# Performance work log

Measured on AMD Instinct MI355X. Metric: run time of the kernel, lower is better.

## Reference

```python
import jax, jax.numpy as jnp
import numpy as np

# Dims: tokens [B,H,W,C]; 3x3 local window (NB=9 neighbors); relative-pos embed dim RP.
B, H, W, C = 4, 96, 96, 128
K, NB, RP = 3, 9, 8
HID = 128              # edge_hidden_dim = max(hidden_dim//2=128, feature_dim=128)
EDGE_IN = 3 * C + RP   # [center, neighbor, center-neighbor, rel_pos] -> 392
CLIP = 3.0
GATE_EPS = 1e-6
LN_EPS = 1e-5


def _ln(x, w, b):
    m = jnp.mean(x, axis=-1, keepdims=True)
    v = jnp.mean((x - m) ** 2, axis=-1, keepdims=True)
    return (x - m) * jax.lax.rsqrt(v + LN_EPS) * w + b


def _mlp(x, w1, b1, w2, b2):
    # Linear -> GELU (exact/erf, torch default) -> Linear; dropout is identity in eval mode.
    return jax.nn.gelu(x @ w1 + b1, approximate=False) @ w2 + b2


def _eml(drive, resistance, gamma_raw, lam, bias, warmup_eta):
    # EMLUnit energy gate (source not provided; Ohm's-law style drive/resistance,
    # positive resistance via softplus, clipped, warmup-scaled, learned bias).
    gamma = jax.nn.softplus(gamma_raw)
    conduct = drive / (jax.nn.softplus(resistance) + gamma + GATE_EPS)
    return warmup_eta * jnp.clip(lam * conduct, -CLIP, CLIP) + bias


def setup_inputs() -> dict:
    key = jax.random.key(0)
    ks = jax.random.split(key, 8)

    def w(k, shape, std=0.01):
        return jax.random.normal(k, shape, jnp.float32) * std

    return {
        "tokens": jax.random.normal(ks[0], (B, H, W, C), jnp.float32),
        "ln1_w": jnp.ones((C,), jnp.float32), "ln1_b": jnp.zeros((C,), jnp.float32),
        "ln2_w": jnp.ones((C,), jnp.float32), "ln2_b": jnp.zeros((C,), jnp.float32),
        "rel_pos": w(ks[1], (NB, RP), 0.02),
        "d_w1": w(ks[2], (EDGE_IN, HID)), "d_b1": jnp.zeros((HID,), jnp.float32),
        "d_w2": w(ks[3], (HID, 1)), "d_b2": jnp.zeros((1,), jnp.float32),
        "r_w1": w(ks[4], (EDGE_IN, HID)), "r_b1": jnp.zeros((HID,), jnp.float32),
        "r_w2": w(ks[5], (HID, 1)), "r_b2": jnp.zeros((1,), jnp.float32),
        "v_w": w(ks[6], (C, C)), "v_b": jnp.zeros((C,), jnp.float32),
        "o_w": w(ks[7], (C, C)), "o_b": jnp.zeros((C,), jnp.float32),
        "eml_gamma": jnp.full((1,), 0.1, jnp.float32),
        "eml_lam": jnp.ones((1,), jnp.float32),
        "eml_bias": jnp.full((1,), -0.3, jnp.float32),
    }


def reference(tokens, ln1_w, ln1_b, ln2_w, ln2_b, rel_pos,
              d_w1, d_b1, d_w2, d_b2, r_w1, r_b1, r_w2, r_b2,
              v_w, v_b, o_w, o_b, eml_gamma, eml_lam, eml_bias):
    b, h, w_, c = tokens.shape
    hw = h * w_
    norm = _ln(tokens, ln1_w, ln1_b)
    # nn.Unfold(kernel=3, padding=1): zero-pad then gather 3x3 windows (row-major ky,kx order).
    pad = jnp.pad(norm, ((0, 0), (1, 1), (1, 1), (0, 0)))
    neigh = jnp.stack([pad[:, dy:dy + h, dx:dx + w_, :]
                       for dy in range(K) for dx in range(K)], axis=3)  # [B,H,W,9,C]
    neigh = neigh.reshape(b, hw, NB, c)
    center = jnp.broadcast_to(norm.reshape(b, hw, 1, c), (b, hw, NB, c))
    relp = jnp.broadcast_to(rel_pos[None, None], (b, hw, NB, RP))
    edge = jnp.concatenate([center, neigh, center - neigh, relp], axis=-1)  # [B,HW,9,392]
    drive = _mlp(edge, d_w1, d_b1, d_w2, d_b2)[..., 0]        # [B,HW,9]
    resistance = _mlp(edge, r_w1, r_b1, r_w2, r_b2)[..., 0]   # [B,HW,9]
    energy = _eml(drive, resistance, eml_gamma, eml_lam, eml_bias, 1.0)
    gate = jax.nn.sigmoid(energy)[..., None]                  # [B,HW,9,1]
    values = neigh @ v_w + v_b                                # [B,HW,9,C]
    gate_mass = jnp.clip(jnp.sum(gate, axis=2), GATE_EPS, None)  # [B,HW,1]
    message = jnp.sum(gate * values, axis=2) / gate_mass      # [B,HW,C]
    update = (message @ o_w + o_b).reshape(b, h, w_, c)
    return _ln(tokens + update, ln2_w, ln2_b)
```

## Files before the change

kernel.cpp:

```cpp
#include <hip/hip_runtime.h>
#include <stdint.h>

#define NPIX 36864

using bf16x8 = __attribute__((ext_vector_type(8))) short;
using f32x4  = __attribute__((ext_vector_type(4))) float;
using f32x2  = __attribute__((ext_vector_type(2))) float;

__device__ __forceinline__ float bf2f(uint16_t u){
  return __uint_as_float(((uint32_t)u) << 16);
}
__device__ __forceinline__ float bl(uint32_t u){ return __uint_as_float(u << 16); }
__device__ __forceinline__ float bh(uint32_t u){ return __uint_as_float(u & 0xFFFF0000u); }
__device__ __forceinline__ uint16_t f2bf(float f){
  uint32_t u = __float_as_uint(f);
  u += 0x7fffu + ((u >> 16) & 1u);
  return (uint16_t)(u >> 16);
}
__device__ __forceinline__ float ldw(const void* p, int i, bool f32){
  return f32 ? ((const float*)p)[i] : bf2f(((const uint16_t*)p)[i]);
}
__device__ __forceinline__ bool probe_f32(const void* ones_vec){
  return ((const uint32_t*)ones_vec)[0] == 0x3F800000u;
}
__device__ __forceinline__ float softplusf(float x){
  return fmaxf(x, 0.f) + __logf(1.f + __expf(-fabsf(x)));
}
__device__ __forceinline__ f32x2 up2(uint32_t u){
  f32x2 r; r.x = __uint_as_float(u << 16); r.y = __uint_as_float(u & 0xFFFF0000u); return r;
}
__device__ __forceinline__ void sg2(f32x2& acc, uint32_t c, uint32_t n, f32x2 r, f32x2 w){
  f32x2 z = up2(c) + up2(n) + r;
  float sx = __builtin_amdgcn_fmed3f(fmaf(z.x, 0.4255f, 0.5f), 0.f, 1.f);
  float sy = __builtin_amdgcn_fmed3f(fmaf(z.y, 0.4255f, 0.5f), 0.f, 1.f);
  acc.x = fmaf(z.x * sx, w.x, acc.x);
  acc.y = fmaf(z.y * sy, w.y, acc.y);
}

#define LIDX(p, ch) ((p)*128 + ((((ch) >> 3) ^ ((p) & 15)) << 3) + ((ch) & 7))

__global__ __launch_bounds__(256) void pre_kernel(const void* __restrict__ tokens,
                            const void* __restrict__ ln1w, const void* __restrict__ ln1b,
                            const void* __restrict__ dw1, const void* __restrict__ rw1,
                            const void* __restrict__ vw,  const void* __restrict__ relp,
                            const void* __restrict__ db1, const void* __restrict__ rb1,
                            const void* __restrict__ ow,
                            const void* __restrict__ dw2, const void* __restrict__ rw2,
                            const void* __restrict__ vb,  const void* __restrict__ db2,
                            const void* __restrict__ rb2, const void* __restrict__ eg,
                            const void* __restrict__ el,  const void* __restrict__ eb,
                            uint16_t* __restrict__ norm,
                            uint16_t* __restrict__ wcatT, float* __restrict__ Rd,
                            float* __restrict__ Rr, uint16_t* __restrict__ owT,
                            float* __restrict__ w2df, float* __restrict__ w2rf,
                            float* __restrict__ vbf, float* __restrict__ sc){
  const bool F = probe_f32(ln1w);
  const int b = blockIdx.x;
  if (b < NPIX/4){
    const int wv = threadIdx.x >> 6, lane = threadIdx.x & 63;
    const int p = b * 4 + wv;
    float f0, f1;
    if (F){
      const float2 t = ((const float2*)tokens)[(size_t)p*64 + lane];
      f0 = t.x; f1 = t.y;
    } else {
      const uint32_t pk = ((const uint32_t*)tokens)[(size_t)p*64 + lane];
      f0 = bl(pk); f1 = bh(pk);
    }
    float s = f0 + f1;
    #pragma unroll
    for (int m = 1; m < 64; m <<= 1) s += __shfl_xor(s, m, 64);
    const float mean = s * (1.f/128.f);
    const float d0 = f0 - mean, d1 = f1 - mean;
    float q = d0*d0 + d1*d1;
    #pragma unroll
    for (int m = 1; m < 64; m <<= 1) q += __shfl_xor(q, m, 64);
    const float rs = rsqrtf(q * (1.f/128.f) + 1e-5f);
    const float n0 = d0*rs*ldw(ln1w, 2*lane, F)   + ldw(ln1b, 2*lane, F);
    const float n1 = d1*rs*ldw(ln1w, 2*lane+1, F) + ldw(ln1b, 2*lane+1, F);
    ((uint32_t*)(norm + (size_t)p*128))[lane] = (uint32_t)f2bf(n0) | ((uint32_t)f2bf(n1) << 16);
    return;
  }
  const int j = (b - NPIX/4) * 2 + (threadIdx.x >> 7);
  const int c = threadIdx.x & 127;
  if (j < 640){
    float val;
    if (j < 128)      val = ldw(dw1, c*128 + j, F)             + ldw(dw1, (256+c)*128 + j, F);
    else if (j < 256) val = ldw(dw1, (128+c)*128 + (j-128), F) - ldw(dw1, (256+c)*128 + (j-128), F);
    else if (j < 384) val = ldw(rw1, c*128 + (j-256), F)       + ldw(rw1, (256+c)*128 + (j-256), F);
    else if (j < 512) val = ldw(rw1, (128+c)*128 + (j-384), F) - ldw(rw1, (256+c)*128 + (j-384), F);
    else              val = ldw(vw, c*128 + (j-512), F);
    wcatT[j*128 + c] = f2bf(val);
  } else if (j < 649){
    const int k = j - 640;
    float sd = ldw(db1, c, F);
    float sr = ldw(rb1, c, F);
    #pragma unroll
    for (int r = 0; r < 8; ++r){
      float rp = ldw(relp, k*8 + r, F);
      sd += rp * ldw(dw1, (384+r)*128 + c, F);
      sr += rp * ldw(rw1, (384+r)*128 + c, F);
    }
    Rd[k*128 + c] = sd;
    Rr[k*128 + c] = sr;
  } else if (j < 777){
    const int n = j - 649;
    owT[n*128 + c] = f2bf(ldw(ow, c*128 + n, F));
  } else {
    w2df[c] = ldw(dw2, c, F);
    w2rf[c] = ldw(rw2, c, F);
    vbf[c]  = ldw(vb, c, F);
    if (c == 0){
      sc[0] = ldw(db2, 0, F);
      sc[1] = ldw(rb2, 0, F);
      sc[2] = softplusf(ldw(eg, 0, F));
      sc[3] = ldw(el, 0, F);
      sc[4] = ldw(eb, 0, F);
    }
  }
}

__global__ __launch_bounds__(256) void gemm1_kernel(const uint16_t* __restrict__ A,
                                                    const uint16_t* __restrict__ BT,
                                                    uint16_t* __restrict__ PT,
                                                    uint16_t* __restrict__ V){
  __shared__ __align__(16) char smem[49152];
  uint16_t* As = (uint16_t*)smem;
  uint16_t* Bs = (uint16_t*)(smem + 16384);
  const int row0 = blockIdx.x * 64;
  const int s    = blockIdx.y;
  const int t = threadIdx.x;
  #pragma unroll
  for (int i = 0; i < 4; ++i){
    const int cid = t + i*256;
    const int r = cid >> 4, c8 = cid & 15;
    *(uint4*)&As[r*128 + ((c8 ^ (r & 15)) << 3)] = *(const uint4*)&A[(size_t)(row0+r)*128 + c8*8];
  }
  #pragma unroll
  for (int i = 0; i < 8; ++i){
    const int cid = t + i*256;
    const int r = cid >> 4, c8 = cid & 15;
    *(uint4*)&Bs[r*128 + ((c8 ^ (r & 15)) << 3)] = *(const uint4*)&BT[(size_t)(s*128 + r)*128 + c8*8];
  }
  __syncthreads();
  const int wv = t >> 6, lane = t & 63;
  const int wc = wv * 32;
  const int lr = lane & 15, quad = lane >> 4;
  f32x4 acc[4][2] = {};
  #pragma unroll
  for (int kk = 0; kk < 4; ++kk){
    const int chunk = kk*4 + quad;
    bf16x8 a[4], b[2];
    #pragma unroll
    for (int mi = 0; mi < 4; ++mi){
      const int r = mi*16 + lr;
      a[mi] = *(const bf16x8*)&As[r*128 + ((chunk ^ (r & 15)) << 3)];
    }
    #pragma unroll
    for (int ni = 0; ni < 2; ++ni){
      const int r = wc + ni*16 + lr;
      b[ni] = *(const bf16x8*)&Bs[r*128 + ((chunk ^ (r & 15)) << 3)];
    }
    #pragma unroll
    for (int mi = 0; mi < 4; ++mi)
      #pragma unroll
      for (int ni = 0; ni < 2; ++ni)
        acc[mi][ni] = __builtin_amdgcn_mfma_f32_16x16x32_bf16(a[mi], b[ni], acc[mi][ni], 0, 0, 0);
  }
  __syncthreads();
  #pragma unroll
  for (int mi = 0; mi < 4; ++mi){
    #pragma unroll
    for (int ni = 0; ni < 2; ++ni){
      const int ch   = wc + ni*16 + lr;
      const int rowb = mi*16 + quad*4;
      #pragma unroll
      for (int r = 0; r < 4; ++r)
        As[LIDX(rowb + r, ch)] = f2bf(acc[mi][ni][r]);
    }
  }
  __syncthreads();
  uint16_t* const dst = (s == 4) ? V : (PT + (size_t)s * NPIX * 128);
  #pragma unroll
  for (int i = 0; i < 4; ++i){
    const int idx = t + i*256;
    const int c8 = idx & 15, p = idx >> 4;
    const uint4 v = *(const uint4*)&As[p*128 + ((c8 ^ (p & 15)) << 3)];
    ((uint4*)dst)[(size_t)(row0 + p)*16 + c8] = v;
  }
}

__global__ __launch_bounds__(576) void emsg_kernel(
    const uint16_t* __restrict__ PT, const uint16_t* __restrict__ Vg,
    const float* __restrict__ Rd, const float* __restrict__ Rr,
    const float* __restrict__ w2df, const float* __restrict__ w2rf,
    const float* __restrict__ sc, const float* __restrict__ vbf,
    uint16_t* __restrict__ msg){
  __shared__ __align__(16) char smem[79104];
  uint16_t* const PnD = (uint16_t*)smem;
  uint16_t* const PnR = (uint16_t*)(smem + 25600);
  uint16_t* const Vl  = (uint16_t*)(smem + 51200);
  float*    const gl  = (float*)  (smem + 76800);

  const int bid = blockIdx.x;
  const int b   = bid / 144;
  const int tl  = bid - b*144;
  const int ty  = tl / 12;
  const int y0  = ty * 8;
  const int x0  = (tl - ty*12) * 8;
  const int tid = threadIdx.x;

  const uint16_t* const P1 = PT + (size_t)NPIX*128;
  const uint16_t* const P3 = PT + (size_t)3*NPIX*128;

  for (int i = tid; i < 4800; i += 576){
    const int arr = i / 1600;
    const int rem = i - arr*1600;
    const int hq  = rem >> 4;
    const int ch  = rem & 15;
    const int hy  = hq / 10;
    const int hx  = hq - hy*10;
    const int y = y0 - 1 + hy, x = x0 - 1 + hx;
    uint4 v = {0u, 0u, 0u, 0u};
    if (((unsigned)y < 96u) && ((unsigned)x < 96u)){
      const size_t pg = (size_t)((b*96 + y)*96 + x);
      const uint16_t* src = (arr == 0 ? P1 : (arr == 1 ? P3 : Vg)) + pg*128 + ch*8;
      v = *(const uint4*)src;
    }
    if (arr == 2){
      *(uint4*)&Vl[hq*128 + ch*8] = v;
    } else {
      uint16_t* const d = (arr == 0) ? PnD : PnR;
      *(uint4*)((char*)d + hq*256 + ((ch ^ (hq & 15)) << 4)) = v;
    }
  }
  __syncthreads();

  const int wv = tid >> 6, lane = tid & 63;
  const int k  = __builtin_amdgcn_readfirstlane(wv);
  const int ky = k / 3, kx = k - ky*3;
  const int py = lane >> 3, px = lane & 7;
  const int hq = (py + ky)*10 + (px + kx);
  const size_t pg = (size_t)((b*96 + y0 + py)*96 + (x0 + px));
  const float sc0 = sc[0], sc1 = sc[1], sc2 = sc[2], sc3 = sc[3], sc4 = sc[4];
  const char* const nbD = (const char*)PnD + hq*256;
  const char* const nbR = (const char*)PnR + hq*256;
  const int hsw = hq & 15;

  f32x2 ad = {0.f, 0.f};
  {
    const uint4*  Cp = (const uint4*)(PT + pg*128);
    const float4* r4 = (const float4*)(Rd + k*128);
    const float4* w4 = (const float4*)w2df;
    uint4 c = Cp[0];
    uint4 n = *(const uint4*)(nbD + ((0 ^ hsw) << 4));
    #pragma unroll
    for (int i = 0; i < 16; ++i){
      uint4 cn, nn;
      if (i < 15){
        cn = Cp[i+1];
        nn = *(const uint4*)(nbD + (((i+1) ^ hsw) << 4));
      }
      const float4 rA = r4[2*i], rB = r4[2*i+1];
      const float4 wA = w4[2*i], wB = w4[2*i+1];
      sg2(ad, c.x, n.x, f32x2{rA.x, rA.y}, f32x2{wA.x, wA.y});
      sg2(ad, c.y, n.y, f32x2{rA.z, rA.w}, f32x2{wA.z, wA.w});
      sg2(ad, c.z, n.z, f32x2{rB.x, rB.y}, f32x2{wB.x, wB.y});
      sg2(ad, c.w, n.w, f32x2{rB.z, rB.w}, f32x2{wB.z, wB.w});
      c = cn; n = nn;
    }
  }
  f32x2 ar = {0.f, 0.f};
  {
    const uint4*  Cp = (const uint4*)(PT + (size_t)2*NPIX*128 + pg*128);
    const float4* r4 = (const float4*)(Rr + k*128);
    const float4* w4 = (const float4*)w2rf;
    uint4 c = Cp[0];
    uint4 n = *(const uint4*)(nbR + ((0 ^ hsw) << 4));
    #pragma unroll
    for (int i = 0; i < 16; ++i){
      uint4 cn, nn;
      if (i < 15){
        cn = Cp[i+1];
        nn = *(const uint4*)(nbR + (((i+1) ^ hsw) << 4));
      }
      const float4 rA = r4[2*i], rB = r4[2*i+1];
      const float4 wA = w4[2*i], wB = w4[2*i+1];
      sg2(ar, c.x, n.x, f32x2{rA.x, rA.y}, f32x2{wA.x, wA.y});
      sg2(ar, c.y, n.y, f32x2{rA.z, rA.w}, f32x2{wA.z, wA.w});
      sg2(ar, c.z, n.z, f32x2{rB.x, rB.y}, f32x2{wB.x, wB.y});
      sg2(ar, c.w, n.w, f32x2{rB.z, rB.w}, f32x2{wB.z, wB.w});
      c = cn; n = nn;
    }
  }
  const float drive  = (ad.x + ad.y) + sc0;
  const float resist = (ar.x + ar.y) + sc1;
  const float cond = __fdividef(drive, softplusf(resist) + sc2 + 1e-6f);
  const float en = fminf(fmaxf(sc3 * cond, -3.0f), 3.0f) + sc4;
  const float e = __expf(-en);
  gl[k*64 + lane] = __builtin_amdgcn_rcpf(1.0f + e);
  __syncthreads();

  if (wv < 8){
    const float2 vb2 = ((const float2*)vbf)[lane];
    #pragma unroll
    for (int j = 0; j < 8; ++j){
      const int m  = wv*8 + j;
      const int my = m >> 3, mx = m & 7;
      float gk[9], gsum = 0.f;
      #pragma unroll
      for (int kk = 0; kk < 9; ++kk){ gk[kk] = gl[kk*64 + m]; gsum += gk[kk]; }
      float a0 = 0.f, a1 = 0.f;
      #pragma unroll
      for (int kk = 0; kk < 9; ++kk){
        const int kyy = kk / 3;
        const int h2  = (my + kyy)*10 + (mx + kk - kyy*3);
        const uint32_t u = ((const uint32_t*)Vl)[h2*64 + lane];
        a0 = fmaf(gk[kk], bl(u), a0);
        a1 = fmaf(gk[kk], bh(u), a1);
      }
      const float inv = __fdividef(1.0f, fmaxf(gsum, 1e-6f));
      a0 = (a0 + gsum * vb2.x) * inv;
      a1 = (a1 + gsum * vb2.y) * inv;
      const size_t p2 = (size_t)((b*96 + y0 + my)*96 + (x0 + mx));
      ((uint32_t*)msg)[p2*64 + lane] = (uint32_t)f2bf(a0) | ((uint32_t)f2bf(a1) << 16);
    }
  }
}

__global__ __launch_bounds__(256) void out_kernel(const uint16_t* __restrict__ Amsg,
    const uint16_t* __restrict__ owT, const void* __restrict__ tokens,
    const void* __restrict__ ob,  const void* __restrict__ ln2w,
    const void* __restrict__ ln2b, void* __restrict__ out){
  const bool F = probe_f32(ln2w);
  __shared__ __align__(16) char smem[49152];
  uint16_t* Bs = (uint16_t*)smem;
  uint16_t* As = (uint16_t*)(smem + 32768);
  float*    U  = (float*)smem;
  const int row0 = blockIdx.x * 64;
  const int t = threadIdx.x;
  const int wv = t >> 6, lane = t & 63;
  #pragma unroll
  for (int i = 0; i < 8; ++i){
    const int cid = t + i*256;
    const int r = cid >> 4, c8 = cid & 15;
    *(uint4*)&Bs[r*128 + ((c8 ^ (r & 15)) << 3)] = *(const uint4*)&owT[(size_t)r*128 + c8*8];
  }
  #pragma unroll
  for (int i = 0; i < 4; ++i){
    const int cid = t + i*256;
    const int r = cid >> 4, c8 = cid & 15;
    *(uint4*)&As[r*128 + ((c8 ^ (r & 15)) << 3)] = *(const uint4*)&Amsg[(size_t)(row0+r)*128 + c8*8];
  }
  __syncthreads();
  const int wc = wv * 32;
  const int lr = lane & 15, quad = lane >> 4;
  f32x4 acc[4][2] = {};
  #pragma unroll
  for (int kk = 0; kk < 4; ++kk){
    const int chunk = kk*4 + quad;
    bf16x8 a[4], b[2];
    #pragma unroll
    for (int mi = 0; mi < 4; ++mi){
      const int r = mi*16 + lr;
      a[mi] = *(const bf16x8*)&As[r*128 + ((chunk ^ (r & 15)) << 3)];
    }
    #pragma unroll
    for (int ni = 0; ni < 2; ++ni){
      const int r = wc + ni*16 + lr;
      b[ni] = *(const bf16x8*)&Bs[r*128 + ((chunk ^ (r & 15)) << 3)];
    }
    #pragma unroll
    for (int mi = 0; mi < 4; ++mi)
      #pragma unroll
      for (int ni = 0; ni < 2; ++ni)
        acc[mi][ni] = __builtin_amdgcn_mfma_f32_16x16x32_bf16(a[mi], b[ni], acc[mi][ni], 0, 0, 0);
  }
  __syncthreads();
  #pragma unroll
  for (int mi = 0; mi < 4; ++mi)
    #pragma unroll
    for (int ni = 0; ni < 2; ++ni)
      #pragma unroll
      for (int r = 0; r < 4; ++r)
        U[(mi*16 + quad*4 + r)*128 + wc + ni*16 + lr] = acc[mi][ni][r];
  __syncthreads();
  const float lw0 = ldw(ln2w, 2*lane, F), lw1 = ldw(ln2w, 2*lane+1, F);
  const float lb0 = ldw(ln2b, 2*lane, F), lb1 = ldw(ln2b, 2*lane+1, F);
  const float ob0 = ldw(ob, 2*lane, F),   ob1 = ldw(ob, 2*lane+1, F);
  for (int j = 0; j < 16; ++j){
    const int row = wv*16 + j;
    const int p = row0 + row;
    const float2 uv = ((const float2*)U)[row*64 + lane];
    float t0, t1;
    if (F){
      const float2 tk = ((const float2*)tokens)[(size_t)p*64 + lane];
      t0 = tk.x; t1 = tk.y;
    } else {
      const uint32_t tk = ((const uint32_t*)tokens)[(size_t)p*64 + lane];
      t0 = bl(tk); t1 = bh(tk);
    }
    const float a0 = uv.x + ob0 + t0;
    const float a1 = uv.y + ob1 + t1;
    float s = a0 + a1;
    #pragma unroll
    for (int m = 1; m < 64; m <<= 1) s += __shfl_xor(s, m, 64);
    const float mean = s * (1.f/128.f);
    const float d0 = a0 - mean, d1 = a1 - mean;
    float q = d0*d0 + d1*d1;
    #pragma unroll
    for (int m = 1; m < 64; m <<= 1) q += __shfl_xor(q, m, 64);
    const float rs = rsqrtf(q * (1.f/128.f) + 1e-5f);
    const float o0 = d0*rs*lw0 + lb0;
    const float o1 = d1*rs*lw1 + lb1;
    if (F){
      ((float2*)out)[(size_t)p*64 + lane] = make_float2(o0, o1);
    } else {
      ((uint32_t*)out)[(size_t)p*64 + lane] = (uint32_t)f2bf(o0) | ((uint32_t)f2bf(o1) << 16);
    }
  }
}

extern "C" void kernel_launch(void* const* d_in, const int* in_sizes, int n_in,
                              void* d_out, int out_size, void* d_ws, size_t ws_size,
                              hipStream_t stream) {
  const void* tokens = d_in[0];
  const void* ln1w   = d_in[1];
  const void* ln1b   = d_in[2];
  const void* ln2w   = d_in[3];
  const void* ln2b   = d_in[4];
  const void* relp   = d_in[5];
  const void* dw1    = d_in[6];
  const void* db1    = d_in[7];
  const void* dw2    = d_in[8];
  const void* db2    = d_in[9];
  const void* rw1    = d_in[10];
  const void* rb1    = d_in[11];
  const void* rw2    = d_in[12];
  const void* rb2    = d_in[13];
  const void* vw     = d_in[14];
  const void* vb     = d_in[15];
  const void* ow     = d_in[16];
  const void* ob     = d_in[17];
  const void* eg     = d_in[18];
  const void* el     = d_in[19];
  const void* eb     = d_in[20];

  char* ws = (char*)d_ws;
  uint16_t* normb = (uint16_t*)(ws + 0);
  uint16_t* PT    = (uint16_t*)(ws + 9437184);
  uint16_t* V     = (uint16_t*)(ws + 47185920);
  uint16_t* wcatT = (uint16_t*)(ws + 57950208);
  float*    Rd    = (float*)   (ws + 58114048);
  float*    Rr    = (float*)   (ws + 58118656);
  uint16_t* owT   = (uint16_t*)(ws + 58123264);
  float*    w2df  = (float*)   (ws + 58156032);
  float*    w2rf  = (float*)   (ws + 58156544);
  float*    vbf   = (float*)   (ws + 58157056);
  float*    sc    = (float*)   (ws + 58157568);
  uint16_t* msg   = normb;

  pre_kernel<<<NPIX/4 + 389, 256, 0, stream>>>(tokens, ln1w, ln1b,
                                       dw1, rw1, vw, relp, db1, rb1, ow,
                                       dw2, rw2, vb, db2, rb2, eg, el, eb,
                                       normb, wcatT, Rd, Rr, owT, w2df, w2rf, vbf, sc);
  gemm1_kernel<<<dim3(NPIX/64, 5), 256, 0, stream>>>(normb, wcatT, PT, V);
  emsg_kernel<<<576, 576, 0, stream>>>(PT, V, Rd, Rr, w2df, w2rf, sc, vbf, msg);
  out_kernel<<<NPIX/64, 256, 0, stream>>>(msg, owT, tokens, ob, ln2w, ln2b, d_out);
}
```

Baseline: 193.8 us.

## Loop gemm1 over all weight slices per block; read emsg neighbours directly from global

gemm1 now loads the activation tile once and loops over the five weight slices inside a single block, instead of launching a 2D grid that reloads the A tile for every slice. It uses a separate LDS region for the output staging. emsg_kernel no longer stages the neighbour projections in LDS. Each group of 8 lanes handles one pixel, with each lane covering 16 channels, reads centre and neighbour projections straight from global memory, zero-masks out-of-bounds neighbours, and reduces with shuffles. The V halo loads are issued early into registers, and the much smaller LDS footprint allows more resident blocks; the cost is 9x redundant global/L2 reads of the neighbour rows.

```diff
diff --git a/kernel.cpp b/kernel.cpp
--- a/kernel.cpp
+++ b/kernel.cpp
@@ -35,6 +35,9 @@
   float sy = __builtin_amdgcn_fmed3f(fmaf(z.y, 0.4255f, 0.5f), 0.f, 1.f);
   acc.x = fmaf(z.x * sx, w.x, acc.x);
   acc.y = fmaf(z.y * sy, w.y, acc.y);
+}
+__device__ __forceinline__ uint4 m4(uint4 v, uint32_t m){
+  v.x &= m; v.y &= m; v.z &= m; v.w &= m; return v;
 }
 
 #define LIDX(p, ch) ((p)*128 + ((((ch) >> 3) ^ ((p) & 15)) << 3) + ((ch) & 7))
@@ -124,83 +127,82 @@
                                                     const uint16_t* __restrict__ BT,
                                                     uint16_t* __restrict__ PT,
                                                     uint16_t* __restrict__ V){
-  __shared__ __align__(16) char smem[49152];
+  __shared__ __align__(16) char smem[65536];
   uint16_t* As = (uint16_t*)smem;
   uint16_t* Bs = (uint16_t*)(smem + 16384);
+  uint16_t* Cs = (uint16_t*)(smem + 49152);
   const int row0 = blockIdx.x * 64;
-  const int s    = blockIdx.y;
   const int t = threadIdx.x;
+  const int wv = t >> 6, lane = t & 63;
+  const int wc = wv * 32;
+  const int lr = lane & 15, quad = lane >> 4;
   #pragma unroll
   for (int i = 0; i < 4; ++i){
     const int cid = t + i*256;
     const int r = cid >> 4, c8 = cid & 15;
     *(uint4*)&As[r*128 + ((c8 ^ (r & 15)) << 3)] = *(const uint4*)&A[(size_t)(row0+r)*128 + c8*8];
   }
-  #pragma unroll
-  for (int i = 0; i < 8; ++i){
-    const int cid = t + i*256;
-    const int r = cid >> 4, c8 = cid & 15;
-    *(uint4*)&Bs[r*128 + ((c8 ^ (r & 15)) << 3)] = *(const uint4*)&BT[(size_t)(s*128 + r)*128 + c8*8];
-  }
-  __syncthreads();
-  const int wv = t >> 6, lane = t & 63;
-  const int wc = wv * 32;
-  const int lr = lane & 15, quad = lane >> 4;
-  f32x4 acc[4][2] = {};
-  #pragma unroll
-  for (int kk = 0; kk < 4; ++kk){
-    const int chunk = kk*4 + quad;
-    bf16x8 a[4], b[2];
+  for (int s = 0; s < 5; ++s){
+    #pragma unroll
+    for (int i = 0; i < 8; ++i){
+      const int cid = t + i*256;
+      const int r = cid >> 4, c8 = cid & 15;
+      *(uint4*)&Bs[r*128 + ((c8 ^ (r & 15)) << 3)] = *(const uint4*)&BT[(size_t)(s*128 + r)*128 + c8*8];
+    }
+    __syncthreads();
+    f32x4 acc[4][2] = {};
+    #pragma unroll
+    for (int kk = 0; kk < 4; ++kk){
+      const int chunk = kk*4 + quad;
+      bf16x8 a[4], b[2];
+      #pragma unroll
+      for (int mi = 0; mi < 4; ++mi){
+        const int r = mi*16 + lr;
+        a[mi] = *(const bf16x8*)&As[r*128 + ((chunk ^ (r & 15)) << 3)];
+      }
+      #pragma unroll
+      for (int ni = 0; ni < 2; ++ni){
+        const int r = wc + ni*16 + lr;
+        b[ni] = *(const bf16x8*)&Bs[r*128 + ((chunk ^ (r & 15)) << 3)];
+      }
+      #pragma unroll
+      for (int mi = 0; mi < 4; ++mi)
+        #pragma unroll
+        for (int ni = 0; ni < 2; ++ni)
+          acc[mi][ni] = __builtin_amdgcn_mfma_f32_16x16x32_bf16(a[mi], b[ni], acc[mi][ni], 0, 0, 0);
+    }
     #pragma unroll
     for (int mi = 0; mi < 4; ++mi){
-      const int r = mi*16 + lr;
-      a[mi] = *(const bf16x8*)&As[r*128 + ((chunk ^ (r & 15)) << 3)];
-    }
-    #pragma unroll
-    for (int ni = 0; ni < 2; ++ni){
-      const int r = wc + ni*16 + lr;
-      b[ni] = *(const bf16x8*)&Bs[r*128 + ((chunk ^ (r & 15)) << 3)];
-    }
-    #pragma unroll
-    for (int mi = 0; mi < 4; ++mi)
-      #pragma unroll
-      for (int ni = 0; ni < 2; ++ni)
-        acc[mi][ni] = __builtin_amdgcn_mfma_f32_16x16x32_bf16(a[mi], b[ni], acc[mi][ni], 0, 0, 0);
-  }
-  __syncthreads();
-  #pragma unroll
-  for (int mi = 0; mi < 4; ++mi){
-    #pragma unroll
-    for (int ni = 0; ni < 2; ++ni){
-      const int ch   = wc + ni*16 + lr;
-      const int rowb = mi*16 + quad*4;
-      #pragma unroll
-      for (int r = 0; r < 4; ++r)
-        As[LIDX(rowb + r, ch)] = f2bf(acc[mi][ni][r]);
-    }
-  }
-  __syncthreads();
-  uint16_t* const dst = (s == 4) ? V : (PT + (size_t)s * NPIX * 128);
-  #pragma unroll
-  for (int i = 0; i < 4; ++i){
-    const int idx = t + i*256;
-    const int c8 = idx & 15, p = idx >> 4;
-    const uint4 v = *(const uint4*)&As[p*128 + ((c8 ^ (p & 15)) << 3)];
-    ((uint4*)dst)[(size_t)(row0 + p)*16 + c8] = v;
-  }
-}
-
-__global__ __launch_bounds__(576) void emsg_kernel(
+      #pragma unroll
+      for (int ni = 0; ni < 2; ++ni){
+        const int ch   = wc + ni*16 + lr;
+        const int rowb = mi*16 + quad*4;
+        #pragma unroll
+        for (int r = 0; r < 4; ++r)
+          Cs[LIDX(rowb + r, ch)] = f2bf(acc[mi][ni][r]);
+      }
+    }
+    __syncthreads();
+    uint16_t* const dst = (s == 4) ? V : (PT + (size_t)s * NPIX * 128);
+    #pragma unroll
+    for (int i = 0; i < 4; ++i){
+      const int idx = t + i*256;
+      const int c8 = idx & 15, p = idx >> 4;
+      const uint4 v = *(const uint4*)&Cs[p*128 + ((c8 ^ (p & 15)) << 3)];
+      ((uint4*)dst)[(size_t)(row0 + p)*16 + c8] = v;
+    }
+  }
+}
+
+__global__ __launch_bounds__(576, 5) void emsg_kernel(
     const uint16_t* __restrict__ PT, const uint16_t* __restrict__ Vg,
     const float* __restrict__ Rd, const float* __restrict__ Rr,
     const float* __restrict__ w2df, const float* __restrict__ w2rf,
     const float* __restrict__ sc, const float* __restrict__ vbf,
     uint16_t* __restrict__ msg){
-  __shared__ __align__(16) char smem[79104];
-  uint16_t* const PnD = (uint16_t*)smem;
-  uint16_t* const PnR = (uint16_t*)(smem + 25600);
-  uint16_t* const Vl  = (uint16_t*)(smem + 51200);
-  float*    const gl  = (float*)  (smem + 76800);
+  __shared__ __align__(16) char smem[27904];
+  uint16_t* const Vl = (uint16_t*)smem;
+  float*    const gl = (float*)(smem + 25600);
 
   const int bid = blockIdx.x;
   const int b   = bid / 144;
@@ -210,106 +212,115 @@
   const int x0  = (tl - ty*12) * 8;
   const int tid = threadIdx.x;
 
-  const uint16_t* const P1 = PT + (size_t)NPIX*128;
-  const uint16_t* const P3 = PT + (size_t)3*NPIX*128;
-
-  for (int i = tid; i < 4800; i += 576){
-    const int arr = i / 1600;
-    const int rem = i - arr*1600;
-    const int hq  = rem >> 4;
-    const int ch  = rem & 15;
-    const int hy  = hq / 10;
-    const int hx  = hq - hy*10;
-    const int y = y0 - 1 + hy, x = x0 - 1 + hx;
-    uint4 v = {0u, 0u, 0u, 0u};
-    if (((unsigned)y < 96u) && ((unsigned)x < 96u)){
-      const size_t pg = (size_t)((b*96 + y)*96 + x);
-      const uint16_t* src = (arr == 0 ? P1 : (arr == 1 ? P3 : Vg)) + pg*128 + ch*8;
-      v = *(const uint4*)src;
-    }
-    if (arr == 2){
-      *(uint4*)&Vl[hq*128 + ch*8] = v;
-    } else {
-      uint16_t* const d = (arr == 0) ? PnD : PnR;
-      *(uint4*)((char*)d + hq*256 + ((ch ^ (hq & 15)) << 4)) = v;
-    }
-  }
-  __syncthreads();
+  uint4 sv0 = {0,0,0,0}, sv1 = {0,0,0,0}, sv2 = {0,0,0,0};
+  const bool has2 = (tid + 1152) < 1600;
+  {
+    const int i0 = tid, i1 = tid + 576, i2 = tid + 1152;
+    #define LDV(dst, i) { \
+      const int hq = (i) >> 4, ch = (i) & 15; \
+      const int hy = hq / 10, hx = hq - hy*10; \
+      const int y = y0 - 1 + hy, x = x0 - 1 + hx; \
+      if (((unsigned)y < 96u) && ((unsigned)x < 96u)) \
+        dst = *(const uint4*)&Vg[((size_t)((b*96 + y)*96 + x))*128 + ch*8]; }
+    LDV(sv0, i0)
+    LDV(sv1, i1)
+    if (has2) LDV(sv2, i2)
+    #undef LDV
+  }
 
   const int wv = tid >> 6, lane = tid & 63;
   const int k  = __builtin_amdgcn_readfirstlane(wv);
   const int ky = k / 3, kx = k - ky*3;
-  const int py = lane >> 3, px = lane & 7;
-  const int hq = (py + ky)*10 + (px + kx);
-  const size_t pg = (size_t)((b*96 + y0 + py)*96 + (x0 + px));
+  const int dy = ky - 1, dx = kx - 1;
+  const int pl = lane >> 3;
+  const int cg = lane & 7;
   const float sc0 = sc[0], sc1 = sc[1], sc2 = sc[2], sc3 = sc[3], sc4 = sc[4];
-  const char* const nbD = (const char*)PnD + hq*256;
-  const char* const nbR = (const char*)PnR + hq*256;
-  const int hsw = hq & 15;
-
-  f32x2 ad = {0.f, 0.f};
+
+  float4 RD[4], WD[4];
   {
-    const uint4*  Cp = (const uint4*)(PT + pg*128);
-    const float4* r4 = (const float4*)(Rd + k*128);
-    const float4* w4 = (const float4*)w2df;
-    uint4 c = Cp[0];
-    uint4 n = *(const uint4*)(nbD + ((0 ^ hsw) << 4));
-    #pragma unroll
-    for (int i = 0; i < 16; ++i){
-      uint4 cn, nn;
-      if (i < 15){
-        cn = Cp[i+1];
-        nn = *(const uint4*)(nbD + (((i+1) ^ hsw) << 4));
-      }
-      const float4 rA = r4[2*i], rB = r4[2*i+1];
-      const float4 wA = w4[2*i], wB = w4[2*i+1];
-      sg2(ad, c.x, n.x, f32x2{rA.x, rA.y}, f32x2{wA.x, wA.y});
-      sg2(ad, c.y, n.y, f32x2{rA.z, rA.w}, f32x2{wA.z, wA.w});
-      sg2(ad, c.z, n.z, f32x2{rB.x, rB.y}, f32x2{wB.x, wB.y});
-      sg2(ad, c.w, n.w, f32x2{rB.z, rB.w}, f32x2{wB.z, wB.w});
-      c = cn; n = nn;
-    }
-  }
-  f32x2 ar = {0.f, 0.f};
+    const float4* r4 = (const float4*)(Rd + k*128) + cg*4;
+    const float4* w4 = (const float4*)w2df + cg*4;
+    #pragma unroll
+    for (int i = 0; i < 4; ++i){ RD[i] = r4[i]; WD[i] = w4[i]; }
+  }
+  const float4* const r4r = (const float4*)(Rr + k*128) + cg*4;
+  const float4* const w4r = (const float4*)w2rf + cg*4;
+
+  const uint4* const S0 = (const uint4*)PT;
+  const uint4* const S1 = (const uint4*)(PT + (size_t)NPIX*128);
+  const uint4* const S2 = (const uint4*)(PT + (size_t)2*NPIX*128);
+  const uint4* const S3 = (const uint4*)(PT + (size_t)3*NPIX*128);
+
+  const int xn = x0 + pl + dx;
+  const bool xin = ((unsigned)xn < 96u);
+
+  for (int ry = 0; ry < 8; ++ry){
+    const int y = y0 + ry;
+    const int p = (b*96 + y)*96 + x0 + pl;
+    const int yn = y + dy;
+    const bool inb = xin && ((unsigned)yn < 96u);
+    const uint32_t m = inb ? 0xFFFFFFFFu : 0u;
+    const int q = inb ? ((b*96 + yn)*96 + xn) : p;
+    const size_t cb = (size_t)p*16 + cg*2;
+    const size_t nb = (size_t)q*16 + cg*2;
+    const uint4 c0a = S0[cb],   c0b = S0[cb+1];
+    const uint4 n1a = m4(S1[nb], m), n1b = m4(S1[nb+1], m);
+    const uint4 c2a = S2[cb],   c2b = S2[cb+1];
+    const uint4 n3a = m4(S3[nb], m), n3b = m4(S3[nb+1], m);
+
+    f32x2 ad = {0.f, 0.f};
+    sg2(ad, c0a.x, n1a.x, f32x2{RD[0].x, RD[0].y}, f32x2{WD[0].x, WD[0].y});
+    sg2(ad, c0a.y, n1a.y, f32x2{RD[0].z, RD[0].w}, f32x2{WD[0].z, WD[0].w});
+    sg2(ad, c0a.z, n1a.z, f32x2{RD[1].x, RD[1].y}, f32x2{WD[1].x, WD[1].y});
+    sg2(ad, c0a.w, n1a.w, f32x2{RD[1].z, RD[1].w}, f32x2{WD[1].z, WD[1].w});
+    sg2(ad, c0b.x, n1b.x, f32x2{RD[2].x, RD[2].y}, f32x2{WD[2].x, WD[2].y});
+    sg2(ad, c0b.y, n1b.y, f32x2{RD[2].z, RD[2].w}, f32x2{WD[2].z, WD[2].w});
+    sg2(ad, c0b.z, n1b.z, f32x2{RD[3].x, RD[3].y}, f32x2{WD[3].x, WD[3].y});
+    sg2(ad, c0b.w, n1b.w, f32x2{RD[3].z, RD[3].w}, f32x2{WD[3].z, WD[3].w});
+
+    const float4 RRa = r4r[0], RRb = r4r[1], RRc = r4r[2], RRd = r4r[3];
+    const float4 WRa = w4r[0], WRb = w4r[1], WRc = w4r[2], WRd = w4r[3];
+    f32x2 ar = {0.f, 0.f};
+    sg2(ar, c2a.x, n3a.x, f32x2{RRa.x, RRa.y}, f32x2{WRa.x, WRa.y});
+    sg2(ar, c2a.y, n3a.y, f32x2{RRa.z, RRa.w}, f32x2{WRa.z, WRa.w});
+    sg2(ar, c2a.z, n3a.z, f32x2{RRb.x, RRb.y}, f32x2{WRb.x, WRb.y});
+    sg2(ar, c2a.w, n3a.w, f32x2{RRb.z, RRb.w}, f32x2{WRb.z, WRb.w});
+    sg2(ar, c2b.x, n3b.x, f32x2{RRc.x, RRc.y}, f32x2{WRc.x, WRc.y});
+    sg2(ar, c2b.y, n3b.y, f32x2{RRc.z, RRc.w}, f32x2{WRc.z, WRc.w});
+    sg2(ar, c2b.z, n3b.z, f32x2{RRd.x, RRd.y}, f32x2{WRd.x, WRd.y});
+    sg2(ar, c2b.w, n3b.w, f32x2{RRd.z, RRd.w}, f32x2{WRd.z, WRd.w});
+
+    float sd = ad.x + ad.y;
+    float sr = ar.x + ar.y;
+    sd += __shfl_xor(sd, 1, 64); sd += __shfl_xor(sd, 2, 64); sd += __shfl_xor(sd, 4, 64);
+    sr += __shfl_xor(sr, 1, 64); sr += __shfl_xor(sr, 2, 64); sr += __shfl_xor(sr, 4, 64);
+
+    const float drive  = sd + sc0;
+    const float resist = sr + sc1;
+    const float cond = __fdividef(drive, softplusf(resist) + sc2 + 1e-6f);
+    const float en = fminf(fmaxf(sc3 * cond, -3.0f), 3.0f) + sc4;
+    const float e = __expf(-en);
+    const float g = __builtin_amdgcn_rcpf(1.0f + e);
+    if (cg == 0) gl[k*64 + ry*8 + pl] = g;
+  }
+
   {
-    const uint4*  Cp = (const uint4*)(PT + (size_t)2*NPIX*128 + pg*128);
-    const float4* r4 = (const float4*)(Rr + k*128);
-    const float4* w4 = (const float4*)w2rf;
-    uint4 c = Cp[0];
-    uint4 n = *(const uint4*)(nbR + ((0 ^ hsw) << 4));
-    #pragma unroll
-    for (int i = 0; i < 16; ++i){
-      uint4 cn, nn;
-      if (i < 15){
-        cn = Cp[i+1];
-        nn = *(const uint4*)(nbR + (((i+1) ^ hsw) << 4));
-      }
-      const float4 rA = r4[2*i], rB = r4[2*i+1];
-      const float4 wA = w4[2*i], wB = w4[2*i+1];
-      sg2(ar, c.x, n.x, f32x2{rA.x, rA.y}, f32x2{wA.x, wA.y});
-      sg2(ar, c.y, n.y, f32x2{rA.z, rA.w}, f32x2{wA.z, wA.w});
-      sg2(ar, c.z, n.z, f32x2{rB.x, rB.y}, f32x2{wB.x, wB.y});
-      sg2(ar, c.w, n.w, f32x2{rB.z, rB.w}, f32x2{wB.z, wB.w});
-      c = cn; n = nn;
-    }
-  }
-  const float drive  = (ad.x + ad.y) + sc0;
-  const float resist = (ar.x + ar.y) + sc1;
-  const float cond = __fdividef(drive, softplusf(resist) + sc2 + 1e-6f);
-  const float en = fminf(fmaxf(sc3 * cond, -3.0f), 3.0f) + sc4;
-  const float e = __expf(-en);
-  gl[k*64 + lane] = __builtin_amdgcn_rcpf(1.0f + e);
+    const int i0 = tid, i1 = tid + 576, i2 = tid + 1152;
+    *(uint4*)&Vl[(i0 >> 4)*128 + (i0 & 15)*8] = sv0;
+    *(uint4*)&Vl[(i1 >> 4)*128 + (i1 & 15)*8] = sv1;
+    if (has2) *(uint4*)&Vl[(i2 >> 4)*128 + (i2 & 15)*8] = sv2;
+  }
   __syncthreads();
 
   if (wv < 8){
     const float2 vb2 = ((const float2*)vbf)[lane];
     #pragma unroll
     for (int j = 0; j < 8; ++j){
-      const int m  = wv*8 + j;
-      const int my = m >> 3, mx = m & 7;
+      const int mp = wv*8 + j;
+      const int my = mp >> 3, mx = mp & 7;
       float gk[9], gsum = 0.f;
       #pragma unroll
-      for (int kk = 0; kk < 9; ++kk){ gk[kk] = gl[kk*64 + m]; gsum += gk[kk]; }
+      for (int kk = 0; kk < 9; ++kk){ gk[kk] = gl[kk*64 + mp]; gsum += gk[kk]; }
       float a0 = 0.f, a1 = 0.f;
       #pragma unroll
       for (int kk = 0; kk < 9; ++kk){
@@ -464,7 +475,7 @@
                                        dw1, rw1, vw, relp, db1, rb1, ow,
                                        dw2, rw2, vb, db2, rb2, eg, el, eb,
                                        normb, wcatT, Rd, Rr, owT, w2df, w2rf, vbf, sc);
-  gemm1_kernel<<<dim3(NPIX/64, 5), 256, 0, stream>>>(normb, wcatT, PT, V);
+  gemm1_kernel<<<NPIX/64, 256, 0, stream>>>(normb, wcatT, PT, V);
   emsg_kernel<<<576, 576, 0, stream>>>(PT, V, Rd, Rr, w2df, w2rf, sc, vbf, msg);
   out_kernel<<<NPIX/64, 256, 0, stream>>>(msg, owT, tokens, ob, ln2w, ln2b, d_out);
 }
```

After: 234.6 us. 1.21x slower.
